# Kernel optimization log

Hardware: AMD Instinct MI355X
Metric: run time of the kernel (lower is better)

## Reference

```python
import jax, jax.numpy as jnp
import numpy as np

B, T, D, H = 64, 512, 512, 1024
IMG = 2048

def setup_inputs() -> dict:
    key = jax.random.key(0)
    ks = jax.random.split(key, 8)
    s_ih = 1.0 / np.sqrt(H)
    return {
        "x": jax.random.normal(ks[0], (B, T, D), dtype=jnp.float32),
        "img_context": jax.random.normal(ks[1], (B, IMG), dtype=jnp.float32),
        "W_ih": jax.random.uniform(ks[2], (4 * H, D), dtype=jnp.float32, minval=-s_ih, maxval=s_ih),
        "W_hh": jax.random.uniform(ks[3], (4 * H, H), dtype=jnp.float32, minval=-s_ih, maxval=s_ih),
        "b_ih": jax.random.uniform(ks[4], (4 * H,), dtype=jnp.float32, minval=-s_ih, maxval=s_ih),
        "b_hh": jax.random.uniform(ks[5], (4 * H,), dtype=jnp.float32, minval=-s_ih, maxval=s_ih),
        "W_m": jax.random.uniform(ks[6], (H, IMG), dtype=jnp.float32, minval=-1.0/np.sqrt(IMG), maxval=1.0/np.sqrt(IMG)),
    }

def reference(x, img_context, W_ih, W_hh, b_ih, b_hh, W_m):
    hid = W_hh.shape[1]
    # Multimodal gate d = M(img_context); loop-invariant, hoisted out of the scan.
    d = img_context @ W_m.T  # [B, H]
    # Precompute input projections for all timesteps in one GEMM: [T, B, 4H]
    xs = jnp.transpose(x, (1, 0, 2))  # [T, B, D]
    x_proj = jnp.einsum('tbd,gd->tbg', xs, W_ih) + b_ih + b_hh

    def step(carry, xp):
        h, c = carry
        h = h * d  # multimodal gating multiply applied before the cell
        gates = xp + h @ W_hh.T  # [B, 4H]
        i, f, g, o = jnp.split(gates, 4, axis=-1)
        i = jax.nn.sigmoid(i)
        f = jax.nn.sigmoid(f)
        g = jnp.tanh(g)
        o = jax.nn.sigmoid(o)
        c = f * c + i * g
        h = o * jnp.tanh(c)
        return (h, c), h

    h0 = jnp.zeros((x.shape[0], hid), dtype=x.dtype)
    c0 = jnp.zeros((x.shape[0], hid), dtype=x.dtype)
    (hn, cn), outs = jax.lax.scan(step, (h0, c0), x_proj)
    out = jnp.transpose(outs, (1, 0, 2))  # [B, T, H]
    return out, hn, cn
```

## Files before the change

kernel.cpp:

```cpp
#include <hip/hip_runtime.h>
#include <math.h>

constexpr int B_   = 64;
constexpr int T_   = 512;
constexpr int D_   = 512;
constexpr int H_   = 1024;
constexpr int IMG_ = 2048;
constexpr int NWG  = 256;
constexpr int NTHR = 256;

constexpr size_t SLOT_U16   = (size_t)B_ * H_;
constexpr size_t RING_BYTES = (size_t)(T_ + 1) * SLOT_U16 * 2;
constexpr size_t XBF_BYTES  = (size_t)B_ * T_ * D_ * 2;

typedef __attribute__((ext_vector_type(8))) short    short8;
typedef __attribute__((ext_vector_type(4))) float    f32x4;
typedef __attribute__((ext_vector_type(4))) unsigned uint4v;

__device__ __forceinline__ unsigned short f2bf(float f) {
  unsigned u = __float_as_uint(f);
  u += 0x7FFFu + ((u >> 16) & 1u);
  return (unsigned short)(u >> 16);
}
__device__ __forceinline__ float sigf(float v) {
  return __fdividef(1.0f, 1.0f + __expf(-v));
}
__device__ __forceinline__ float tanhfast(float v) {
  v = fminf(15.0f, fmaxf(-15.0f, v));
  const float e = __expf(2.0f * v);
  return __fdividef(e - 1.0f, e + 1.0f);
}
__device__ __forceinline__ short8 pk8(const float4 a, const float4 b) {
  union { unsigned u[4]; short8 s; } r;
  asm("v_cvt_pk_bf16_f32 %0, %1, %2" : "=v"(r.u[0]) : "v"(a.x), "v"(a.y));
  asm("v_cvt_pk_bf16_f32 %0, %1, %2" : "=v"(r.u[1]) : "v"(a.z), "v"(a.w));
  asm("v_cvt_pk_bf16_f32 %0, %1, %2" : "=v"(r.u[2]) : "v"(b.x), "v"(b.y));
  asm("v_cvt_pk_bf16_f32 %0, %1, %2" : "=v"(r.u[3]) : "v"(b.z), "v"(b.w));
  return r.s;
}

__global__ void __launch_bounds__(NTHR)
x_repack_kernel(const float* __restrict__ x, unsigned short* __restrict__ x_bf) {
  const int idx = blockIdx.x * NTHR + threadIdx.x;
  const int k8 = idx & 63;
  const int t  = (idx >> 6) & 511;
  const int b  = idx >> 15;
  const float* px = x + ((size_t)b * T_ + t) * D_ + k8 * 8;
  const float4 v0 = *(const float4*)px;
  const float4 v1 = *(const float4*)(px + 4);
  const size_t off = ((size_t)(t * 4 + (b >> 4)) * 16 + (k8 >> 2)) * 512
                   + (size_t)(k8 & 3) * 128 + (size_t)(b & 15) * 8;
  *(short8*)(x_bf + off) = pk8(v0, v1);
}

template<int RING, int XBF>
__global__ void __launch_bounds__(NTHR, 1)
mmlstm_persistent(const float* __restrict__ x,
                  const unsigned short* __restrict__ x_bf,
                  const float* __restrict__ img,
                  const float* __restrict__ W_ih,
                  const float* __restrict__ W_hh,
                  const float* __restrict__ b_ih,
                  const float* __restrict__ b_hh,
                  const float* __restrict__ W_m,
                  float* __restrict__ out,
                  float* __restrict__ hn,
                  float* __restrict__ cn,
                  unsigned* __restrict__ flags,
                  unsigned short* __restrict__ ring)
{
  __shared__ float gaccs[4][16][68];
  __shared__ float bias_lds[64];
  __shared__ char  ldspad[72 * 1024];

  const int tid  = threadIdx.x;
  const int lane = tid & 63;
  const int wv   = tid >> 6;
  const int wg   = blockIdx.x;
  const int q    = wg & 3;
  const int cgid = wg >> 2;
  const int b0   = q * 16;
  const int j0   = cgid * 16;

  ((volatile char*)ldspad)[tid] = 0;

  unsigned* myflags = flags + q * 64;
  unsigned* myslot  = myflags + cgid;

  const int cloc = lane & 15;
  const int ko8  = (lane >> 4) << 3;
  short8 wx[4][4], wh[4][8];
  #pragma unroll
  for (int tile = 0; tile < 4; ++tile) {
    const int grow = tile * H_ + j0 + cloc;
    #pragma unroll
    for (int sx = 0; sx < 4; ++sx) {
      const float* p = W_ih + (size_t)grow * D_ + (wv + 4 * sx) * 32 + ko8;
      wx[tile][sx] = pk8(*(const float4*)p, *(const float4*)(p + 4));
    }
    #pragma unroll
    for (int sh = 0; sh < 8; ++sh) {
      const float* p = W_hh + (size_t)grow * H_ + (wv + 4 * sh) * 32 + ko8;
      wh[tile][sh] = pk8(*(const float4*)p, *(const float4*)(p + 4));
    }
  }
  if (tid < 64) {
    const int grow = (tid >> 4) * H_ + j0 + (tid & 15);
    bias_lds[tid] = b_ih[grow] + b_hh[grow];
  }

  const int b_l = tid >> 4;
  const int jj  = tid & 15;
  const int b   = b0 + b_l;
  const int j   = j0 + jj;

  const int poff = (j >> 5) * 512 + ((j >> 3) & 3) * 128 + b_l * 8 + (j & 7);

  float dval = 0.0f;
  {
    const float4* ir = (const float4*)(img + (size_t)b * IMG_);
    const float4* wr = (const float4*)(W_m + (size_t)j * IMG_);
    for (int k = 0; k < IMG_ / 4; ++k) {
      const float4 a = ir[k];
      const float4 w = wr[k];
      dval += a.x * w.x + a.y * w.y + a.z * w.z + a.w * w.w;
    }
  }

  if ((jj & 1) == 0)
    __hip_atomic_store((unsigned*)(ring + (size_t)q * 16384 + poff), 0u,
                       __ATOMIC_RELAXED, __HIP_MEMORY_SCOPE_AGENT);

  float cstate = 0.0f;

  __syncthreads();
  if (tid == 0)
    __hip_atomic_store(myslot, 1u, __ATOMIC_RELAXED, __HIP_MEMORY_SCOPE_AGENT);

  auto poll = [&](unsigned target) {
    for (;;) {
      const unsigned f = __hip_atomic_load(myflags + lane, __ATOMIC_RELAXED,
                                           __HIP_MEMORY_SCOPE_AGENT);
      if (__all(f >= target)) break;
    }
  };

  short8 xr[4];
  auto xprefetch = [&](int t) {
    if (XBF) {
      const unsigned short* xb = x_bf + ((size_t)t * 4 + q) * 8192;
      #pragma unroll
      for (int sx = 0; sx < 4; ++sx)
        xr[sx] = *(const short8*)(xb + (size_t)(wv + 4 * sx) * 512 + lane * 8);
    } else {
      const float* rb = x + ((size_t)(b0 + cloc) * T_ + t) * D_ + ko8;
      #pragma unroll
      for (int sx = 0; sx < 4; ++sx) {
        const float* p = rb + (wv + 4 * sx) * 32;
        xr[sx] = pk8(*(const float4*)p, *(const float4*)(p + 4));
      }
    }
  };

  xprefetch(0);

  for (int t = 0; t < T_; ++t) {
    poll((unsigned)(t + 1));
    asm volatile("" ::: "memory");

    const unsigned short* sp = ring + (size_t)(RING ? t : (t & 1)) * SLOT_U16
                             + (size_t)q * 16384;
    short8 hfr[8];
    if (RING) {
      #pragma unroll
      for (int sh = 0; sh < 8; ++sh)
        hfr[sh] = *(const short8*)(sp + (size_t)(wv + 4 * sh) * 512 + lane * 8);
    } else {
      uint4v tmp[8];
      #pragma unroll
      for (int sh = 0; sh < 8; ++sh) {
        const unsigned short* ap = sp + (size_t)(wv + 4 * sh) * 512 + lane * 8;
        asm volatile("global_load_dwordx4 %0, %1, off sc0 sc1" : "=&v"(tmp[sh]) : "v"(ap));
      }
      asm volatile("s_waitcnt vmcnt(0)" ::: "memory");
      __builtin_amdgcn_sched_barrier(0);
      #pragma unroll
      for (int sh = 0; sh < 8; ++sh)
        hfr[sh] = *(short8*)&tmp[sh];
    }

    f32x4 ac[4];
    #pragma unroll
    for (int tile = 0; tile < 4; ++tile) ac[tile] = (f32x4){0.f, 0.f, 0.f, 0.f};
    #pragma unroll
    for (int sx = 0; sx < 4; ++sx) {
      #pragma unroll
      for (int tile = 0; tile < 4; ++tile)
        ac[tile] = __builtin_amdgcn_mfma_f32_16x16x32_bf16(xr[sx], wx[tile][sx], ac[tile], 0, 0, 0);
    }
    #pragma unroll
    for (int sh = 0; sh < 8; ++sh) {
      #pragma unroll
      for (int tile = 0; tile < 4; ++tile)
        ac[tile] = __builtin_amdgcn_mfma_f32_16x16x32_bf16(hfr[sh], wh[tile][sh], ac[tile], 0, 0, 0);
    }

    {
      const int crow = (lane >> 4) * 4;
      #pragma unroll
      for (int tile = 0; tile < 4; ++tile) {
        #pragma unroll
        for (int rr = 0; rr < 4; ++rr)
          gaccs[wv][crow + rr][tile * 16 + cloc] = ac[tile][rr];
      }
    }
    __syncthreads();

    float gv[4];
    #pragma unroll
    for (int g = 0; g < 4; ++g) {
      const int c = g * 16 + jj;
      gv[g] = gaccs[0][b_l][c] + gaccs[1][b_l][c] + gaccs[2][b_l][c] + gaccs[3][b_l][c]
            + bias_lds[c];
    }
    const float ig = sigf(gv[0]);
    const float fg = sigf(gv[1]);
    const float gg = tanhfast(gv[2]);
    const float og = sigf(gv[3]);
    cstate = fg * cstate + ig * gg;
    const float h = og * tanhfast(cstate);

    {
      const unsigned hd  = f2bf(h * dval);
      const unsigned nxt = __shfl_down((int)hd, 1);
      if ((jj & 1) == 0)
        __hip_atomic_store((unsigned*)(ring + (size_t)(RING ? (t + 1) : ((t + 1) & 1)) * SLOT_U16
                                       + (size_t)q * 16384 + poff),
                           hd | (nxt << 16),
                           __ATOMIC_RELAXED, __HIP_MEMORY_SCOPE_AGENT);
    }
    __syncthreads();
    if (t < T_ - 1 && tid == 0)
      __hip_atomic_store(myslot, (unsigned)(t + 2), __ATOMIC_RELAXED, __HIP_MEMORY_SCOPE_AGENT);

    __builtin_nontemporal_store(h, &out[((size_t)b * T_ + t) * H_ + j]);
    if (t == T_ - 1) {
      hn[(size_t)b * H_ + j] = h;
      cn[(size_t)b * H_ + j] = cstate;
    } else {
      xprefetch(t + 1);
    }
  }
}

extern "C" void kernel_launch(void* const* d_in, const int* in_sizes, int n_in,
                              void* d_out, int out_size, void* d_ws, size_t ws_size,
                              hipStream_t stream) {
  (void)in_sizes; (void)n_in; (void)out_size;
  const float* x    = (const float*)d_in[0];
  const float* img  = (const float*)d_in[1];
  const float* W_ih = (const float*)d_in[2];
  const float* W_hh = (const float*)d_in[3];
  const float* b_ih = (const float*)d_in[4];
  const float* b_hh = (const float*)d_in[5];
  const float* W_m  = (const float*)d_in[6];

  float* out = (float*)d_out;
  float* hn  = out + (size_t)B_ * T_ * H_;
  float* cn  = hn + (size_t)B_ * H_;

  unsigned*       flags = (unsigned*)d_ws;
  unsigned short* ring  = (unsigned short*)((char*)d_ws + 4096);
  unsigned short* x_bf  = (unsigned short*)((char*)d_ws + 4096 + RING_BYTES);

  hipMemsetAsync(d_ws, 0, 4096, stream);

  if (ws_size >= 4096 + RING_BYTES + XBF_BYTES) {
    hipLaunchKernelGGL(x_repack_kernel, dim3((B_ * T_ * D_ / 8) / NTHR), dim3(NTHR), 0, stream,
                       x, x_bf);
    hipLaunchKernelGGL((mmlstm_persistent<1, 1>), dim3(NWG), dim3(NTHR), 0, stream,
                       x, x_bf, img, W_ih, W_hh, b_ih, b_hh, W_m, out, hn, cn, flags, ring);
  } else if (ws_size >= 4096 + RING_BYTES) {
    hipLaunchKernelGGL((mmlstm_persistent<1, 0>), dim3(NWG), dim3(NTHR), 0, stream,
                       x, x_bf, img, W_ih, W_hh, b_ih, b_hh, W_m, out, hn, cn, flags, ring);
  } else {
    hipLaunchKernelGGL((mmlstm_persistent<0, 0>), dim3(NWG), dim3(NTHR), 0, stream,
                       x, x_bf, img, W_ih, W_hh, b_ih, b_hh, W_m, out, hn, cn, flags, ring);
  }
}
```

Measured before the change: 1.541 ms.

## Replace flag polling with sentinel-filled ring data polling in persistent LSTM

```diff
diff --git a/kernel.cpp b/kernel.cpp
--- a/kernel.cpp
+++ b/kernel.cpp
@@ -12,6 +12,7 @@
 constexpr size_t SLOT_U16   = (size_t)B_ * H_;
 constexpr size_t RING_BYTES = (size_t)(T_ + 1) * SLOT_U16 * 2;
 constexpr size_t XBF_BYTES  = (size_t)B_ * T_ * D_ * 2;
+constexpr unsigned SENT32   = 0x7F7F7F7Fu;
 
 typedef __attribute__((ext_vector_type(8))) short    short8;
 typedef __attribute__((ext_vector_type(4))) float    f32x4;
@@ -134,10 +135,10 @@
   float cstate = 0.0f;
 
   __syncthreads();
-  if (tid == 0)
+  if (RING == 0 && tid == 0)
     __hip_atomic_store(myslot, 1u, __ATOMIC_RELAXED, __HIP_MEMORY_SCOPE_AGENT);
 
-  auto poll = [&](unsigned target) {
+  auto pollFlags = [&](unsigned target) {
     for (;;) {
       const unsigned f = __hip_atomic_load(myflags + lane, __ATOMIC_RELAXED,
                                            __HIP_MEMORY_SCOPE_AGENT);
@@ -165,17 +166,35 @@
   xprefetch(0);
 
   for (int t = 0; t < T_; ++t) {
-    poll((unsigned)(t + 1));
-    asm volatile("" ::: "memory");
-
     const unsigned short* sp = ring + (size_t)(RING ? t : (t & 1)) * SLOT_U16
                              + (size_t)q * 16384;
     short8 hfr[8];
     if (RING) {
-      #pragma unroll
-      for (int sh = 0; sh < 8; ++sh)
-        hfr[sh] = *(const short8*)(sp + (size_t)(wv + 4 * sh) * 512 + lane * 8);
+      for (;;) {
+        uint4v tmp[8];
+        #pragma unroll
+        for (int sh = 0; sh < 8; ++sh) {
+          const unsigned short* ap = sp + (size_t)(wv + 4 * sh) * 512 + lane * 8;
+          asm volatile("global_load_dwordx4 %0, %1, off sc0 sc1"
+                       : "=&v"(tmp[sh]) : "v"(ap));
+        }
+        asm volatile("s_waitcnt vmcnt(0)" ::: "memory");
+        __builtin_amdgcn_sched_barrier(0);
+        bool ok = true;
+        #pragma unroll
+        for (int sh = 0; sh < 8; ++sh)
+          #pragma unroll
+          for (int e = 0; e < 4; ++e)
+            ok &= (tmp[sh][e] != SENT32);
+        if (__all(ok)) {
+          #pragma unroll
+          for (int sh = 0; sh < 8; ++sh) hfr[sh] = *(short8*)&tmp[sh];
+          break;
+        }
+      }
     } else {
+      pollFlags((unsigned)(t + 1));
+      asm volatile("" ::: "memory");
       uint4v tmp[8];
       #pragma unroll
       for (int sh = 0; sh < 8; ++sh) {
@@ -214,7 +233,9 @@
           gaccs[wv][crow + rr][tile * 16 + cloc] = ac[tile][rr];
       }
     }
-    __syncthreads();
+    asm volatile("s_waitcnt lgkmcnt(0)" ::: "memory");
+    __builtin_amdgcn_s_barrier();
+    __builtin_amdgcn_sched_barrier(0);
 
     float gv[4];
     #pragma unroll
@@ -239,9 +260,15 @@
                            hd | (nxt << 16),
                            __ATOMIC_RELAXED, __HIP_MEMORY_SCOPE_AGENT);
     }
-    __syncthreads();
-    if (t < T_ - 1 && tid == 0)
-      __hip_atomic_store(myslot, (unsigned)(t + 2), __ATOMIC_RELAXED, __HIP_MEMORY_SCOPE_AGENT);
+
+    if (RING) {
+      __builtin_amdgcn_s_barrier();
+      __builtin_amdgcn_sched_barrier(0);
+    } else {
+      __syncthreads();
+      if (t < T_ - 1 && tid == 0)
+        __hip_atomic_store(myslot, (unsigned)(t + 2), __ATOMIC_RELAXED, __HIP_MEMORY_SCOPE_AGENT);
+    }
 
     __builtin_nontemporal_store(h, &out[((size_t)b * T_ + t) * H_ + j]);
     if (t == T_ - 1) {
@@ -276,11 +303,13 @@
   hipMemsetAsync(d_ws, 0, 4096, stream);
 
   if (ws_size >= 4096 + RING_BYTES + XBF_BYTES) {
+    hipMemsetAsync(ring, 0x7F, RING_BYTES, stream);
     hipLaunchKernelGGL(x_repack_kernel, dim3((B_ * T_ * D_ / 8) / NTHR), dim3(NTHR), 0, stream,
                        x, x_bf);
     hipLaunchKernelGGL((mmlstm_persistent<1, 1>), dim3(NWG), dim3(NTHR), 0, stream,
                        x, x_bf, img, W_ih, W_hh, b_ih, b_hh, W_m, out, hn, cn, flags, ring);
   } else if (ws_size >= 4096 + RING_BYTES) {
+    hipMemsetAsync(ring, 0x7F, RING_BYTES, stream);
     hipLaunchKernelGGL((mmlstm_persistent<1, 0>), dim3(NWG), dim3(NTHR), 0, stream,
                        x, x_bf, img, W_ih, W_hh, b_ih, b_hh, W_m, out, hn, cn, flags, ring);
   } else {
```

Measured after the change: 1.324 ms. 14.1% less time.
